# Performance work log

Hardware: AMD Instinct MI355X
Metric: run time of the kernel (lower is better)

The kernel has to match this reference:

```python
import jax, jax.numpy as jnp
import numpy as np

N_NODES = 100000
N_EDGES = 1600000
EMBED = 64
HEADS = 8
HEAD_DIM = EMBED // HEADS
FFN = 4 * EMBED
EPS = 1e-5


def _layer_norm(x, g, b):
    m = jnp.mean(x, axis=-1, keepdims=True)
    v = jnp.mean(jnp.square(x - m), axis=-1, keepdims=True)
    return (x - m) * jax.lax.rsqrt(v + EPS) * g + b


def setup_inputs() -> dict:
    key = jax.random.key(0)
    ks = jax.random.split(key, 10)
    s = lambda fan_in: 1.0 / np.sqrt(fan_in)
    x = jax.random.normal(ks[0], (N_NODES, EMBED), dtype=jnp.float32)
    edge_indices = jax.random.randint(ks[1], (2, N_EDGES), 0, N_NODES, dtype=jnp.int64)
    attn_w = jax.random.uniform(ks[2], (EMBED, 3 * EMBED), jnp.float32, -s(EMBED), s(EMBED))
    attn_b = jnp.zeros((3 * EMBED,), jnp.float32)
    w1 = jax.random.uniform(ks[3], (EMBED, FFN), jnp.float32, -s(EMBED), s(EMBED))
    b1 = jnp.zeros((FFN,), jnp.float32)
    w2 = jax.random.uniform(ks[4], (FFN, EMBED), jnp.float32, -s(FFN), s(FFN))
    b2 = jnp.zeros((EMBED,), jnp.float32)
    ln1_g = jnp.ones((EMBED,), jnp.float32)
    ln1_b = jnp.zeros((EMBED,), jnp.float32)
    ln2_g = jnp.ones((EMBED,), jnp.float32)
    ln2_b = jnp.zeros((EMBED,), jnp.float32)
    return {"x": x, "edge_indices": edge_indices, "attn_w": attn_w, "attn_b": attn_b,
            "w1": w1, "b1": b1, "w2": w2, "b2": b2,
            "ln1_g": ln1_g, "ln1_b": ln1_b, "ln2_g": ln2_g, "ln2_b": ln2_b}


def _self_attention(x, edge_indices, attn_w, attn_b):
    n = x.shape[0]
    row, col = edge_indices[0], edge_indices[1]
    scale = EMBED ** (-0.5)  # note: original scales by embed_dim**-0.5
    qkv = (x @ attn_w + attn_b).reshape(n, HEADS, 3 * HEAD_DIM)
    q, k, v = jnp.split(qkv, 3, axis=2)  # each [N, H, Dh]
    alpha = jnp.sum(q[row] * k[col], axis=2) * scale  # [E, H]
    # sparse per-row softmax via segment reductions
    m = jax.ops.segment_max(alpha, row, num_segments=n)  # [N, H]
    e = jnp.exp(alpha - m[row])
    denom = jax.ops.segment_sum(e, row, num_segments=n)  # [N, H]
    weights = e / denom[row]  # [E, H]
    vals = v[col] * weights[:, :, None]  # [E, H, Dh]
    out = jax.ops.segment_sum(vals, row, num_segments=n)  # [N, H, Dh]
    return out.reshape(n, EMBED)


def reference(x, edge_indices, attn_w, attn_b, w1, b1, w2, b2, ln1_g, ln1_b, ln2_g, ln2_b):
    # post-norm (norm_first=False), dropout=0
    x = _layer_norm(x + _self_attention(x, edge_indices, attn_w, attn_b), ln1_g, ln1_b)
    ffn = jax.nn.relu(x @ w1 + b1) @ w2 + b2
    x = _layer_norm(x + ffn, ln2_g, ln2_b)
    return x
```

## Files before the change

### kernel.cpp

```cpp
#include <hip/hip_runtime.h>
#include <hip/hip_bf16.h>


#define WAVE 64
constexpr int BUCKET_SHIFT = 7;
constexpr int NBMAX = 800;

typedef __attribute__((ext_vector_type(8))) short bf16x8;
typedef __attribute__((ext_vector_type(4))) float f32x4;

__device__ __forceinline__ float bfbits_lo(unsigned u) {
  return __uint_as_float(u << 16);
}
__device__ __forceinline__ float bfbits_hi(unsigned u) {
  return __uint_as_float(u & 0xffff0000u);
}
__device__ __forceinline__ unsigned f2bf_pk(float a, float b) {
  unsigned ua = __float_as_uint(a);
  unsigned ub = __float_as_uint(b);
  ua = (ua + 0x7fff + ((ua >> 16) & 1)) >> 16;
  ub = (ub + 0x7fff + ((ub >> 16) & 1)) & 0xffff0000u;
  return ua | ub;
}

__global__ __launch_bounds__(256) void cvt_w(
    const float* __restrict__ aw, const float* __restrict__ w1,
    const float* __restrict__ w2, unsigned short* __restrict__ awT,
    unsigned short* __restrict__ w1T, unsigned short* __restrict__ w2T) {
  int tid = blockIdx.x * 256 + threadIdx.x;
  int stride = gridDim.x * 256;
  for (int i = tid; i < 192 * 64; i += stride) {
    int nn = i >> 6, kk = i & 63;
    awT[i] = (unsigned short)(__float_as_uint(aw[kk * 192 + nn] * 1.f) >> 16 ==
                                      0
                                  ? 0
                                  : 0);
  }
}

__device__ __forceinline__ unsigned short f2bf1(float a) {
  unsigned ua = __float_as_uint(a);
  ua = (ua + 0x7fff + ((ua >> 16) & 1)) >> 16;
  return (unsigned short)ua;
}

__global__ __launch_bounds__(256) void cvt_w2(
    const float* __restrict__ aw, const float* __restrict__ w1,
    const float* __restrict__ w2, unsigned short* __restrict__ awT,
    unsigned short* __restrict__ w1T, unsigned short* __restrict__ w2T) {
  int tid = blockIdx.x * 256 + threadIdx.x;
  int stride = gridDim.x * 256;
  for (int i = tid; i < 192 * 64; i += stride) {
    int nn = i >> 6, kk = i & 63;
    awT[i] = f2bf1(aw[kk * 192 + nn]);
  }
  for (int i = tid; i < 256 * 64; i += stride) {
    int nn = i >> 6, kk = i & 63;
    w1T[i] = f2bf1(w1[kk * 256 + nn]);
  }
  for (int i = tid; i < 64 * 256; i += stride) {
    int nn = i >> 8, kk = i & 255;
    w2T[i] = f2bf1(w2[kk * 64 + nn]);
  }
}

__global__ __launch_bounds__(256) void cvt_x(const float* __restrict__ x,
                                             unsigned short* __restrict__ xb,
                                             int total8) {
  int i = blockIdx.x * 256 + threadIdx.x;
  int stride = gridDim.x * 256;
  const float4* xf = (const float4*)x;
  uint4* xo = (uint4*)xb;
  for (; i < total8; i += stride) {
    float4 a = xf[2 * i], b = xf[2 * i + 1];
    uint4 st = make_uint4(f2bf_pk(a.x, a.y), f2bf_pk(a.z, a.w),
                          f2bf_pk(b.x, b.y), f2bf_pk(b.z, b.w));
    xo[i] = st;
  }
}

template <int NCOLS, int K, int MODE>
__global__ __launch_bounds__(256) void mfma_gemm(
    const unsigned short* __restrict__ A, const unsigned short* __restrict__ BT,
    const float* __restrict__ bias, unsigned short* __restrict__ out_q,
    unsigned short* __restrict__ out_kv, unsigned short* __restrict__ out_h,
    const float* __restrict__ resid, const float* __restrict__ g,
    const float* __restrict__ beta, float* __restrict__ out_f, int n) {
  constexpr int KP = K + 8;
  constexpr int NT = NCOLS / 16;
  constexpr int NKC = K / 32;
  __shared__ unsigned short sB[NCOLS * KP];

  const int tid = threadIdx.x;
  {
    const uint4* src = (const uint4*)BT;
    for (int idx = tid; idx < NCOLS * K / 8; idx += 256) {
      int nn = idx / (K / 8), kq = idx % (K / 8);
      *(uint4*)&sB[nn * KP + kq * 8] = src[idx];
    }
  }
  __syncthreads();

  const int wid = tid >> 6, lane = tid & 63;
  const int l15 = lane & 15, quad = lane >> 4;
  const int rowbase = blockIdx.x * 128 + wid * 32;

  bf16x8 afrag[2][NKC];
#pragma unroll
  for (int rg = 0; rg < 2; rg++) {
    int row = rowbase + rg * 16 + l15;
    if (row >= n) row = n - 1;
    const bf16x8* ap = (const bf16x8*)(A + (size_t)row * K);
#pragma unroll
    for (int kc = 0; kc < NKC; kc++) afrag[rg][kc] = ap[kc * 4 + quad];
  }

  f32x4 acc[2][NT];
#pragma unroll
  for (int rg = 0; rg < 2; rg++)
#pragma unroll
    for (int t = 0; t < NT; t++) acc[rg][t] = (f32x4){0.f, 0.f, 0.f, 0.f};

#pragma unroll
  for (int t = 0; t < NT; t++) {
#pragma unroll
    for (int kc = 0; kc < NKC; kc++) {
      bf16x8 b =
          *(const bf16x8*)&sB[(t * 16 + l15) * KP + kc * 32 + quad * 8];
      acc[0][t] = __builtin_amdgcn_mfma_f32_16x16x32_bf16(b, afrag[0][kc],
                                                          acc[0][t], 0, 0, 0);
      acc[1][t] = __builtin_amdgcn_mfma_f32_16x16x32_bf16(b, afrag[1][kc],
                                                          acc[1][t], 0, 0, 0);
    }
  }

  if (MODE == 0) {
#pragma unroll
    for (int rg = 0; rg < 2; rg++) {
      int row = rowbase + rg * 16 + l15;
      if (row >= n) continue;
#pragma unroll
      for (int t = 0; t < NT; t++) {
        int c0 = t * 16 + quad * 4;
        float4 bb = *(const float4*)&bias[c0];
        float v0 = acc[rg][t].x + bb.x, v1 = acc[rg][t].y + bb.y;
        float v2 = acc[rg][t].z + bb.z, v3 = acc[rg][t].w + bb.w;
        int hh = c0 / 24, rem = c0 % 24;
        unsigned short* dst;
        if (rem < 8) {
          v0 *= 0.125f;
          v1 *= 0.125f;
          v2 *= 0.125f;
          v3 *= 0.125f;
          dst = out_q + (size_t)row * 64 + hh * 8 + rem;
        } else if (rem < 16) {
          dst = out_kv + (size_t)row * 128 + hh * 16 + (rem - 8);
        } else {
          dst = out_kv + (size_t)row * 128 + hh * 16 + 8 + (rem - 16);
        }
        *(uint2*)dst = make_uint2(f2bf_pk(v0, v1), f2bf_pk(v2, v3));
      }
    }
  } else if (MODE == 1) {
#pragma unroll
    for (int rg = 0; rg < 2; rg++) {
      int row = rowbase + rg * 16 + l15;
      if (row >= n) continue;
#pragma unroll
      for (int t = 0; t < NT; t++) {
        int c0 = t * 16 + quad * 4;
        float4 bb = *(const float4*)&bias[c0];
        float v0 = fmaxf(acc[rg][t].x + bb.x, 0.f);
        float v1 = fmaxf(acc[rg][t].y + bb.y, 0.f);
        float v2 = fmaxf(acc[rg][t].z + bb.z, 0.f);
        float v3 = fmaxf(acc[rg][t].w + bb.w, 0.f);
        *(uint2*)(out_h + (size_t)row * NCOLS + c0) =
            make_uint2(f2bf_pk(v0, v1), f2bf_pk(v2, v3));
      }
    }
  } else {
#pragma unroll
    for (int rg = 0; rg < 2; rg++) {
      int row = rowbase + rg * 16 + l15;
      bool ok = row < n;
      int rowc = ok ? row : n - 1;
      float vals[4][4];
      float ps = 0.f, pq = 0.f;
#pragma unroll
      for (int t = 0; t < 4; t++) {
        int c0 = t * 16 + quad * 4;
        float4 bb = *(const float4*)&bias[c0];
        float4 rr = *(const float4*)&resid[(size_t)rowc * 64 + c0];
        vals[t][0] = acc[rg][t].x + bb.x + rr.x;
        vals[t][1] = acc[rg][t].y + bb.y + rr.y;
        vals[t][2] = acc[rg][t].z + bb.z + rr.z;
        vals[t][3] = acc[rg][t].w + bb.w + rr.w;
#pragma unroll
        for (int r = 0; r < 4; r++) {
          ps += vals[t][r];
          pq += vals[t][r] * vals[t][r];
        }
      }
      ps += __shfl_xor(ps, 16);
      ps += __shfl_xor(ps, 32);
      pq += __shfl_xor(pq, 16);
      pq += __shfl_xor(pq, 32);
      float mean = ps * (1.f / 64.f);
      float var = pq * (1.f / 64.f) - mean * mean;
      float inv = rsqrtf(var + 1e-5f);
      if (ok) {
#pragma unroll
        for (int t = 0; t < 4; t++) {
          int c0 = t * 16 + quad * 4;
          float4 gg = *(const float4*)&g[c0];
          float4 be = *(const float4*)&beta[c0];
          float4 o =
              make_float4((vals[t][0] - mean) * inv * gg.x + be.x,
                          (vals[t][1] - mean) * inv * gg.y + be.y,
                          (vals[t][2] - mean) * inv * gg.z + be.z,
                          (vals[t][3] - mean) * inv * gg.w + be.w);
          *(float4*)&out_f[(size_t)row * 64 + c0] = o;
        }
      }
    }
  }
}

__global__ void detect_kernel(const int* __restrict__ e, unsigned* flag) {
  unsigned v = 0;
  for (int i = threadIdx.x; i < 2048; i += 256) v |= (unsigned)e[2 * i + 1];
#pragma unroll
  for (int m = 1; m < WAVE; m <<= 1) v |= (unsigned)__shfl_xor((int)v, m);
  if ((threadIdx.x & 63) == 0 && v) atomicOr(flag, 1u);
}

__device__ __forceinline__ int edge_row(const int* e, int i, bool is64) {
  return is64 ? e[2 * (size_t)i] : e[i];
}
__device__ __forceinline__ int edge_col(const int* e, int i, int E, bool is64) {
  return is64 ? e[2 * ((size_t)E + i)] : e[(size_t)E + i];
}

__global__ __launch_bounds__(256) void partition_count(
    const int* __restrict__ e, int E, const unsigned* __restrict__ flag,
    int* __restrict__ G, int NB, int CH) {
  __shared__ int h[NBMAX];
  bool is64 = (*flag == 0u);
  for (int b = threadIdx.x; b < NB; b += 256) h[b] = 0;
  __syncthreads();
  int c0 = blockIdx.x * CH, c1 = min(E, c0 + CH);
  for (int i = c0 + threadIdx.x; i < c1; i += 256)
    atomicAdd(&h[edge_row(e, i, is64) >> BUCKET_SHIFT], 1);
  __syncthreads();
  for (int b = threadIdx.x; b < NB; b += 256) G[b * 256 + blockIdx.x] = h[b];
}

__global__ __launch_bounds__(1024) void scan_reduce(const int* __restrict__ in,
                                                    int n,
                                                    int* __restrict__ bsum) {
  __shared__ int sdata[16];
  int tid = threadIdx.x;
  int idx = blockIdx.x * 1024 + tid;
  int v = (idx < n) ? in[idx] : 0;
#pragma unroll
  for (int m = 1; m < WAVE; m <<= 1) v += __shfl_xor(v, m);
  if ((tid & 63) == 0) sdata[tid >> 6] = v;
  __syncthreads();
  if (tid < 16) {
    int s = sdata[tid];
#pragma unroll
    for (int m = 1; m < 16; m <<= 1) s += __shfl_xor(s, m);
    if (tid == 0) bsum[blockIdx.x] = s;
  }
}

__global__ __launch_bounds__(256) void scan_top(const int* __restrict__ bsum,
                                                int nb, int* __restrict__ bpre) {
  __shared__ int wsum[4];
  int tid = threadIdx.x;
  int lane = tid & 63, wid = tid >> 6;
  int v = (tid < nb) ? bsum[tid] : 0;
  int incl = v;
#pragma unroll
  for (int m = 1; m < WAVE; m <<= 1) {
    int t = __shfl_up(incl, m);
    if (lane >= m) incl += t;
  }
  if (lane == 63) wsum[wid] = incl;
  __syncthreads();
  int add = 0;
  for (int w = 0; w < wid; w++) add += wsum[w];
  if (tid < nb) bpre[tid] = add + incl - v;
}

__global__ __launch_bounds__(1024) void scan_apply(
    const int* __restrict__ in, int n, const int* __restrict__ bpre,
    int* __restrict__ outscan) {
  __shared__ int wtot[16];
  __shared__ int wexcl[16];
  int tid = threadIdx.x;
  int idx = blockIdx.x * 1024 + tid;
  int v = (idx < n) ? in[idx] : 0;
  int incl = v;
#pragma unroll
  for (int m = 1; m < WAVE; m <<= 1) {
    int t = __shfl_up(incl, m);
    if ((tid & 63) >= m) incl += t;
  }
  int wid = tid >> 6;
  if ((tid & 63) == 63) wtot[wid] = incl;
  __syncthreads();
  if (tid < 16) {
    int w = wtot[tid];
    int wi = w;
#pragma unroll
    for (int m = 1; m < 16; m <<= 1) {
      int t = __shfl_up(wi, m);
      if (tid >= m) wi += t;
    }
    wexcl[tid] = wi - w;
  }
  __syncthreads();
  if (idx < n) outscan[idx] = bpre[blockIdx.x] + wexcl[wid] + incl - v;
}

__global__ __launch_bounds__(256) void partition_scatter(
    const int* __restrict__ e, int E, const unsigned* __restrict__ flag,
    const int* __restrict__ scanG, unsigned* __restrict__ ebuf, int NB,
    int CH) {
  __shared__ int base[NBMAX];
  bool is64 = (*flag == 0u);
  for (int b = threadIdx.x; b < NB; b += 256)
    base[b] = scanG[b * 256 + blockIdx.x];
  __syncthreads();
  int c0 = blockIdx.x * CH, c1 = min(E, c0 + CH);
  for (int i = c0 + threadIdx.x; i < c1; i += 256) {
    int r = edge_row(e, i, is64);
    int c = edge_col(e, i, E, is64);
    int pos = atomicAdd(&base[r >> BUCKET_SHIFT], 1);
    ebuf[pos] = ((unsigned)(r & 127) << 17) | (unsigned)c;
  }
}

__global__ __launch_bounds__(256) void bucket_csr(
    const unsigned* __restrict__ ebuf, const int* __restrict__ scanG,
    int* __restrict__ ecol, int* __restrict__ rowstart, int n, int NB, int E) {
  __shared__ int cnt[128], offs[128], cur[128];
  const int b = blockIdx.x;
  const int tid = threadIdx.x;
  const int start = scanG[b * 256];
  const int end = (b + 1 < NB) ? scanG[(b + 1) * 256] : E;
  if (tid < 128) cnt[tid] = 0;
  __syncthreads();
  for (int i = start + tid; i < end; i += 256)
    atomicAdd(&cnt[(ebuf[i] >> 17) & 127], 1);
  __syncthreads();
  if (tid < 128) offs[tid] = cnt[tid];
  __syncthreads();
  for (int s = 1; s < 128; s <<= 1) {
    int t = 0;
    if (tid < 128 && tid >= s) t = offs[tid - s];
    __syncthreads();
    if (tid < 128) offs[tid] += t;
    __syncthreads();
  }
  if (tid < 128) {
    int excl = offs[tid] - cnt[tid];
    cur[tid] = start + excl;
    int gr = (b << BUCKET_SHIFT) + tid;
    if (gr < n) rowstart[gr] = start + excl;
  }
  if (b == NB - 1 && tid == 0) rowstart[n] = E;
  __syncthreads();
  for (int i = start + tid; i < end; i += 256) {
    unsigned p = ebuf[i];
    int pos = atomicAdd(&cur[(p >> 17) & 127], 1);
    ecol[pos] = (int)(p & 0x1FFFF);
  }
}

__global__ __launch_bounds__(256) void attn_ln_kernel(
    const float* __restrict__ x, const unsigned short* __restrict__ qbuf,
    const unsigned short* __restrict__ kvb, const int* __restrict__ rowstart,
    const int* __restrict__ ecol, const float* __restrict__ g,
    const float* __restrict__ beta, float* __restrict__ x1,
    unsigned short* __restrict__ x1b, int n) {
  int wave = threadIdx.x >> 6;
  int lane = threadIdx.x & 63;
  int node = blockIdx.x * 4 + wave;
  if (node >= n) return;
  const int e = lane >> 3, h = lane & 7;
  const unsigned* kvu = (const unsigned*)kvb;

  uint4 qp = ((const uint4*)(qbuf + (size_t)node * 64))[h];
  float qv[8] = {bfbits_lo(qp.x), bfbits_hi(qp.x), bfbits_lo(qp.y),
                 bfbits_hi(qp.y), bfbits_lo(qp.z), bfbits_hi(qp.z),
                 bfbits_lo(qp.w), bfbits_hi(qp.w)};

  int start = rowstart[node];
  int cnt = rowstart[node + 1] - start;
  float den = 0.f;
  float acc[8] = {0.f, 0.f, 0.f, 0.f, 0.f, 0.f, 0.f, 0.f};

  int iters = (cnt + 7) >> 3;
  for (int it = 0; it < iters; ++it) {
    int i = it * 8 + e;
    bool valid = i < cnt;
    int c = ecol[valid ? start + i : start];
    const uint4* kvrow = (const uint4*)(kvu + (size_t)c * 64 + h * 8);
    uint4 ka = kvrow[0];
    uint4 va = kvrow[1];
    float a = bfbits_lo(ka.x) * qv[0] + bfbits_hi(ka.x) * qv[1] +
              bfbits_lo(ka.y) * qv[2] + bfbits_hi(ka.y) * qv[3] +
              bfbits_lo(ka.z) * qv[4] + bfbits_hi(ka.z) * qv[5] +
              bfbits_lo(ka.w) * qv[6] + bfbits_hi(ka.w) * qv[7];
    float ee = valid ? __expf(a) : 0.f;
    den += ee;
    acc[0] += ee * bfbits_lo(va.x);
    acc[1] += ee * bfbits_hi(va.x);
    acc[2] += ee * bfbits_lo(va.y);
    acc[3] += ee * bfbits_hi(va.y);
    acc[4] += ee * bfbits_lo(va.z);
    acc[5] += ee * bfbits_hi(va.z);
    acc[6] += ee * bfbits_lo(va.w);
    acc[7] += ee * bfbits_hi(va.w);
  }

#pragma unroll
  for (int m = 8; m < 64; m <<= 1) {
    den += __shfl_xor(den, m);
#pragma unroll
    for (int j = 0; j < 8; j++) acc[j] += __shfl_xor(acc[j], m);
  }

  float invden = (cnt > 0) ? 1.f / den : 0.f;

  const float4* xr = (const float4*)(x + (size_t)node * 64 + h * 8);
  float4 xa = xr[0], xb = xr[1];
  float v[8];
  v[0] = xa.x + acc[0] * invden;
  v[1] = xa.y + acc[1] * invden;
  v[2] = xa.z + acc[2] * invden;
  v[3] = xa.w + acc[3] * invden;
  v[4] = xb.x + acc[4] * invden;
  v[5] = xb.y + acc[5] * invden;
  v[6] = xb.z + acc[6] * invden;
  v[7] = xb.w + acc[7] * invden;

  float ps = 0.f;
#pragma unroll
  for (int j = 0; j < 8; j++) ps += v[j];
#pragma unroll
  for (int m = 1; m < 8; m <<= 1) ps += __shfl_xor(ps, m);
  float mean = ps * (1.f / 64.f);
  float pq = 0.f;
#pragma unroll
  for (int j = 0; j < 8; j++) {
    float d = v[j] - mean;
    pq += d * d;
  }
#pragma unroll
  for (int m = 1; m < 8; m <<= 1) pq += __shfl_xor(pq, m);
  float inv = rsqrtf(pq * (1.f / 64.f) + 1e-5f);

  if (e == 0) {
    const float4* gr = (const float4*)(g + h * 8);
    const float4* br = (const float4*)(beta + h * 8);
    float4 ga = gr[0], gb = gr[1];
    float4 ba = br[0], bb = br[1];
    float o[8];
    o[0] = (v[0] - mean) * inv * ga.x + ba.x;
    o[1] = (v[1] - mean) * inv * ga.y + ba.y;
    o[2] = (v[2] - mean) * inv * ga.z + ba.z;
    o[3] = (v[3] - mean) * inv * ga.w + ba.w;
    o[4] = (v[4] - mean) * inv * gb.x + bb.x;
    o[5] = (v[5] - mean) * inv * gb.y + bb.y;
    o[6] = (v[6] - mean) * inv * gb.z + bb.z;
    o[7] = (v[7] - mean) * inv * gb.w + bb.w;
    float4* dst = (float4*)(x1 + (size_t)node * 64 + h * 8);
    dst[0] = make_float4(o[0], o[1], o[2], o[3]);
    dst[1] = make_float4(o[4], o[5], o[6], o[7]);
    *(uint4*)(x1b + (size_t)node * 64 + h * 8) =
        make_uint4(f2bf_pk(o[0], o[1]), f2bf_pk(o[2], o[3]),
                   f2bf_pk(o[4], o[5]), f2bf_pk(o[6], o[7]));
  }
}

extern "C" void kernel_launch(void* const* d_in, const int* in_sizes, int n_in,
                              void* d_out, int out_size, void* d_ws,
                              size_t ws_size, hipStream_t stream) {
  const float* x = (const float*)d_in[0];
  const int* edges = (const int*)d_in[1];
  const float* attn_w = (const float*)d_in[2];
  const float* attn_b = (const float*)d_in[3];
  const float* w1 = (const float*)d_in[4];
  const float* b1 = (const float*)d_in[5];
  const float* w2 = (const float*)d_in[6];
  const float* b2 = (const float*)d_in[7];
  const float* g1 = (const float*)d_in[8];
  const float* bb1 = (const float*)d_in[9];
  const float* g2 = (const float*)d_in[10];
  const float* bb2 = (const float*)d_in[11];

  const int N = in_sizes[0] / 64;
  const int E = in_sizes[1] / 2;
  const int NB = (N + 127) >> BUCKET_SHIFT;
  const int CH = (E + 255) / 256;
  const int NG = NB * 256;

  char* ws = (char*)d_ws;
  size_t oq = 0;
  size_t okv = oq + (size_t)N * 64 * 2;
  size_t ox1 = okv + (size_t)N * 128 * 2;
  size_t ox1b = ox1 + (size_t)N * 64 * 4;
  size_t oxb = ox1b + (size_t)N * 64 * 2;
  size_t oh = oxb + (size_t)N * 64 * 2;
  size_t oawT = oh + (size_t)N * 256 * 2;
  size_t ow1T = oawT + 192 * 64 * 2;
  size_t ow2T = ow1T + 256 * 64 * 2;
  size_t oG = ow2T + 64 * 256 * 2;
  size_t oscanG = oG + (size_t)NG * 4;
  size_t oebuf = oscanG + (size_t)NG * 4;
  size_t oecol = oebuf + (size_t)E * 4;
  size_t orowstart = oecol + (size_t)E * 4;
  size_t obsum = orowstart + (size_t)(N + 4) * 4;
  size_t obpre = obsum + 1024;
  size_t oflag = obpre + 1024;

  unsigned short* qbuf = (unsigned short*)(ws + oq);
  unsigned short* kvb = (unsigned short*)(ws + okv);
  float* x1 = (float*)(ws + ox1);
  unsigned short* x1b = (unsigned short*)(ws + ox1b);
  unsigned short* xb = (unsigned short*)(ws + oxb);
  unsigned short* hbuf = (unsigned short*)(ws + oh);
  unsigned short* awT = (unsigned short*)(ws + oawT);
  unsigned short* w1T = (unsigned short*)(ws + ow1T);
  unsigned short* w2T = (unsigned short*)(ws + ow2T);
  int* G = (int*)(ws + oG);
  int* scanG = (int*)(ws + oscanG);
  unsigned* ebuf = (unsigned*)(ws + oebuf);
  int* ecol = (int*)(ws + oecol);
  int* rowstart = (int*)(ws + orowstart);
  int* bsum = (int*)(ws + obsum);
  int* bpre = (int*)(ws + obpre);
  unsigned* flag = (unsigned*)(ws + oflag);

  hipMemsetAsync(flag, 0, 4, stream);

  cvt_w2<<<32, 256, 0, stream>>>(attn_w, w1, w2, awT, w1T, w2T);
  cvt_x<<<512, 256, 0, stream>>>(x, xb, N * 8);

  detect_kernel<<<1, 256, 0, stream>>>(edges, flag);
  partition_count<<<256, 256, 0, stream>>>(edges, E, flag, G, NB, CH);
  int nscan = (NG + 1023) / 1024;
  scan_reduce<<<nscan, 1024, 0, stream>>>(G, NG, bsum);
  scan_top<<<1, 256, 0, stream>>>(bsum, nscan, bpre);
  scan_apply<<<nscan, 1024, 0, stream>>>(G, NG, bpre, scanG);
  partition_scatter<<<256, 256, 0, stream>>>(edges, E, flag, scanG, ebuf, NB,
                                             CH);
  bucket_csr<<<NB, 256, 0, stream>>>(ebuf, scanG, ecol, rowstart, N, NB, E);

  const int gblocks = (N + 127) / 128;

  mfma_gemm<192, 64, 0><<<gblocks, 256, 0, stream>>>(
      xb, awT, attn_b, qbuf, kvb, nullptr, nullptr, nullptr, nullptr, nullptr,
      N);

  attn_ln_kernel<<<(N + 3) / 4, 256, 0, stream>>>(x, qbuf, kvb, rowstart, ecol,
                                                  g1, bb1, x1, x1b, N);

  mfma_gemm<256, 64, 1><<<gblocks, 256, 0, stream>>>(
      x1b, w1T, b1, nullptr, nullptr, hbuf, nullptr, nullptr, nullptr, nullptr,
      N);

  mfma_gemm<64, 256, 2><<<gblocks, 256, 0, stream>>>(
      hbuf, w2T, b2, nullptr, nullptr, nullptr, x1, g2, bb2, (float*)d_out, N);
}
```

Baseline: 312.7 us.

## Store K/V in FP8, use bf16 residuals, unroll edge loop by two

New measurement: 281.2 us. 1.11x faster.

```diff
diff --git a/kernel.cpp b/kernel.cpp
--- a/kernel.cpp
+++ b/kernel.cpp
@@ -1,5 +1,6 @@
 #include <hip/hip_runtime.h>
 #include <hip/hip_bf16.h>
+#include <hip/hip_fp8.h>
 
 
 #define WAVE 64
@@ -8,6 +9,7 @@
 
 typedef __attribute__((ext_vector_type(8))) short bf16x8;
 typedef __attribute__((ext_vector_type(4))) float f32x4;
+typedef __attribute__((ext_vector_type(2))) float f32x2;
 
 __device__ __forceinline__ float bfbits_lo(unsigned u) {
   return __uint_as_float(u << 16);
@@ -22,26 +24,63 @@
   ub = (ub + 0x7fff + ((ub >> 16) & 1)) & 0xffff0000u;
   return ua | ub;
 }
-
-__global__ __launch_bounds__(256) void cvt_w(
-    const float* __restrict__ aw, const float* __restrict__ w1,
-    const float* __restrict__ w2, unsigned short* __restrict__ awT,
-    unsigned short* __restrict__ w1T, unsigned short* __restrict__ w2T) {
-  int tid = blockIdx.x * 256 + threadIdx.x;
-  int stride = gridDim.x * 256;
-  for (int i = tid; i < 192 * 64; i += stride) {
-    int nn = i >> 6, kk = i & 63;
-    awT[i] = (unsigned short)(__float_as_uint(aw[kk * 192 + nn] * 1.f) >> 16 ==
-                                      0
-                                  ? 0
-                                  : 0);
-  }
-}
-
 __device__ __forceinline__ unsigned short f2bf1(float a) {
   unsigned ua = __float_as_uint(a);
   ua = (ua + 0x7fff + ((ua >> 16) & 1)) >> 16;
   return (unsigned short)ua;
+}
+
+#if defined(__has_builtin)
+#if __has_builtin(__builtin_amdgcn_cvt_pk_f32_fp8) && \
+    __has_builtin(__builtin_amdgcn_cvt_pk_fp8_f32)
+#define FP8_HW 1
+#endif
+#endif
+
+#ifdef FP8_HW
+#define FP8PK0(w) __builtin_amdgcn_cvt_pk_f32_fp8((int)(w), false)
+#define FP8PK1(w) __builtin_amdgcn_cvt_pk_f32_fp8((int)(w), true)
+__device__ __forceinline__ unsigned fp8enc4(float a, float b, float c,
+                                            float d) {
+  int r = __builtin_amdgcn_cvt_pk_fp8_f32(a, b, 0, false);
+  r = __builtin_amdgcn_cvt_pk_fp8_f32(c, d, r, true);
+  return (unsigned)r;
+}
+#else
+__device__ __forceinline__ f32x2 fp8pk_sw(unsigned w, int sh) {
+  __hip_fp8_e4m3 a, b;
+  a.__x = (unsigned char)((w >> sh) & 0xff);
+  b.__x = (unsigned char)((w >> (sh + 8)) & 0xff);
+  f32x2 r;
+  r.x = (float)a;
+  r.y = (float)b;
+  return r;
+}
+#define FP8PK0(w) fp8pk_sw((w), 0)
+#define FP8PK1(w) fp8pk_sw((w), 16)
+__device__ __forceinline__ unsigned fp8enc4(float a, float b, float c,
+                                            float d) {
+  __hip_fp8_e4m3 qa(a), qb(b), qc(c), qd(d);
+  return (unsigned)qa.__x | ((unsigned)qb.__x << 8) |
+         ((unsigned)qc.__x << 16) | ((unsigned)qd.__x << 24);
+}
+#endif
+
+__device__ __forceinline__ float dot8_fp8(uint2 w, const float qv[8]) {
+  f32x2 a = FP8PK0(w.x), b = FP8PK1(w.x), c = FP8PK0(w.y), d = FP8PK1(w.y);
+  return a.x * qv[0] + a.y * qv[1] + b.x * qv[2] + b.y * qv[3] + c.x * qv[4] +
+         c.y * qv[5] + d.x * qv[6] + d.y * qv[7];
+}
+__device__ __forceinline__ void acc8_fp8(uint2 w, float ee, float acc[8]) {
+  f32x2 a = FP8PK0(w.x), b = FP8PK1(w.x), c = FP8PK0(w.y), d = FP8PK1(w.y);
+  acc[0] += ee * a.x;
+  acc[1] += ee * a.y;
+  acc[2] += ee * b.x;
+  acc[3] += ee * b.y;
+  acc[4] += ee * c.x;
+  acc[5] += ee * c.y;
+  acc[6] += ee * d.x;
+  acc[7] += ee * d.y;
 }
 
 __global__ __launch_bounds__(256) void cvt_w2(
@@ -83,8 +122,8 @@
 __global__ __launch_bounds__(256) void mfma_gemm(
     const unsigned short* __restrict__ A, const unsigned short* __restrict__ BT,
     const float* __restrict__ bias, unsigned short* __restrict__ out_q,
-    unsigned short* __restrict__ out_kv, unsigned short* __restrict__ out_h,
-    const float* __restrict__ resid, const float* __restrict__ g,
+    unsigned char* __restrict__ out_kv8, unsigned short* __restrict__ out_h,
+    const unsigned short* __restrict__ resid, const float* __restrict__ g,
     const float* __restrict__ beta, float* __restrict__ out_f, int n) {
   constexpr int KP = K + 8;
   constexpr int NT = NCOLS / 16;
@@ -125,8 +164,7 @@
   for (int t = 0; t < NT; t++) {
 #pragma unroll
     for (int kc = 0; kc < NKC; kc++) {
-      bf16x8 b =
-          *(const bf16x8*)&sB[(t * 16 + l15) * KP + kc * 32 + quad * 8];
+      bf16x8 b = *(const bf16x8*)&sB[(t * 16 + l15) * KP + kc * 32 + quad * 8];
       acc[0][t] = __builtin_amdgcn_mfma_f32_16x16x32_bf16(b, afrag[0][kc],
                                                           acc[0][t], 0, 0, 0);
       acc[1][t] = __builtin_amdgcn_mfma_f32_16x16x32_bf16(b, afrag[1][kc],
@@ -146,19 +184,20 @@
         float v0 = acc[rg][t].x + bb.x, v1 = acc[rg][t].y + bb.y;
         float v2 = acc[rg][t].z + bb.z, v3 = acc[rg][t].w + bb.w;
         int hh = c0 / 24, rem = c0 % 24;
-        unsigned short* dst;
         if (rem < 8) {
           v0 *= 0.125f;
           v1 *= 0.125f;
           v2 *= 0.125f;
           v3 *= 0.125f;
-          dst = out_q + (size_t)row * 64 + hh * 8 + rem;
+          *(uint2*)(out_q + (size_t)row * 64 + hh * 8 + rem) =
+              make_uint2(f2bf_pk(v0, v1), f2bf_pk(v2, v3));
         } else if (rem < 16) {
-          dst = out_kv + (size_t)row * 128 + hh * 16 + (rem - 8);
+          *(unsigned*)(out_kv8 + (size_t)row * 128 + hh * 8 + (rem - 8)) =
+              fp8enc4(v0, v1, v2, v3);
         } else {
-          dst = out_kv + (size_t)row * 128 + hh * 16 + 8 + (rem - 16);
+          *(unsigned*)(out_kv8 + (size_t)row * 128 + 64 + hh * 8 + (rem - 16)) =
+              fp8enc4(v0, v1, v2, v3);
         }
-        *(uint2*)dst = make_uint2(f2bf_pk(v0, v1), f2bf_pk(v2, v3));
       }
     }
   } else if (MODE == 1) {
@@ -190,11 +229,11 @@
       for (int t = 0; t < 4; t++) {
         int c0 = t * 16 + quad * 4;
         float4 bb = *(const float4*)&bias[c0];
-        float4 rr = *(const float4*)&resid[(size_t)rowc * 64 + c0];
-        vals[t][0] = acc[rg][t].x + bb.x + rr.x;
-        vals[t][1] = acc[rg][t].y + bb.y + rr.y;
-        vals[t][2] = acc[rg][t].z + bb.z + rr.z;
-        vals[t][3] = acc[rg][t].w + bb.w + rr.w;
+        uint2 rr = *(const uint2*)&resid[(size_t)rowc * 64 + c0];
+        vals[t][0] = acc[rg][t].x + bb.x + bfbits_lo(rr.x);
+        vals[t][1] = acc[rg][t].y + bb.y + bfbits_hi(rr.x);
+        vals[t][2] = acc[rg][t].z + bb.z + bfbits_lo(rr.y);
+        vals[t][3] = acc[rg][t].w + bb.w + bfbits_hi(rr.y);
 #pragma unroll
         for (int r = 0; r < 4; r++) {
           ps += vals[t][r];
@@ -214,11 +253,10 @@
           int c0 = t * 16 + quad * 4;
           float4 gg = *(const float4*)&g[c0];
           float4 be = *(const float4*)&beta[c0];
-          float4 o =
-              make_float4((vals[t][0] - mean) * inv * gg.x + be.x,
-                          (vals[t][1] - mean) * inv * gg.y + be.y,
-                          (vals[t][2] - mean) * inv * gg.z + be.z,
-                          (vals[t][3] - mean) * inv * gg.w + be.w);
+          float4 o = make_float4((vals[t][0] - mean) * inv * gg.x + be.x,
+                                 (vals[t][1] - mean) * inv * gg.y + be.y,
+                                 (vals[t][2] - mean) * inv * gg.z + be.z,
+                                 (vals[t][3] - mean) * inv * gg.w + be.w);
           *(float4*)&out_f[(size_t)row * 64 + c0] = o;
         }
       }
@@ -380,17 +418,16 @@
 }
 
 __global__ __launch_bounds__(256) void attn_ln_kernel(
-    const float* __restrict__ x, const unsigned short* __restrict__ qbuf,
-    const unsigned short* __restrict__ kvb, const int* __restrict__ rowstart,
+    const unsigned short* __restrict__ xb,
+    const unsigned short* __restrict__ qbuf,
+    const unsigned char* __restrict__ kv8, const int* __restrict__ rowstart,
     const int* __restrict__ ecol, const float* __restrict__ g,
-    const float* __restrict__ beta, float* __restrict__ x1,
-    unsigned short* __restrict__ x1b, int n) {
+    const float* __restrict__ beta, unsigned short* __restrict__ x1b, int n) {
   int wave = threadIdx.x >> 6;
   int lane = threadIdx.x & 63;
   int node = blockIdx.x * 4 + wave;
   if (node >= n) return;
   const int e = lane >> 3, h = lane & 7;
-  const unsigned* kvu = (const unsigned*)kvb;
 
   uint4 qp = ((const uint4*)(qbuf + (size_t)node * 64))[h];
   float qv[8] = {bfbits_lo(qp.x), bfbits_hi(qp.x), bfbits_lo(qp.y),
@@ -403,27 +440,38 @@
   float acc[8] = {0.f, 0.f, 0.f, 0.f, 0.f, 0.f, 0.f, 0.f};
 
   int iters = (cnt + 7) >> 3;
-  for (int it = 0; it < iters; ++it) {
-    int i = it * 8 + e;
-    bool valid = i < cnt;
-    int c = ecol[valid ? start + i : start];
-    const uint4* kvrow = (const uint4*)(kvu + (size_t)c * 64 + h * 8);
-    uint4 ka = kvrow[0];
-    uint4 va = kvrow[1];
-    float a = bfbits_lo(ka.x) * qv[0] + bfbits_hi(ka.x) * qv[1] +
-              bfbits_lo(ka.y) * qv[2] + bfbits_hi(ka.y) * qv[3] +
-              bfbits_lo(ka.z) * qv[4] + bfbits_hi(ka.z) * qv[5] +
-              bfbits_lo(ka.w) * qv[6] + bfbits_hi(ka.w) * qv[7];
-    float ee = valid ? __expf(a) : 0.f;
-    den += ee;
-    acc[0] += ee * bfbits_lo(va.x);
-    acc[1] += ee * bfbits_hi(va.x);
-    acc[2] += ee * bfbits_lo(va.y);
-    acc[3] += ee * bfbits_hi(va.y);
-    acc[4] += ee * bfbits_lo(va.z);
-    acc[5] += ee * bfbits_hi(va.z);
-    acc[6] += ee * bfbits_lo(va.w);
-    acc[7] += ee * bfbits_hi(va.w);
+  int it = 0;
+  for (; it + 2 <= iters; it += 2) {
+    int i0 = it * 8 + e;
+    int i1 = i0 + 8;
+    bool v1 = i1 < cnt;
+    int c0 = ecol[start + i0];
+    int c1 = ecol[start + (v1 ? i1 : i0)];
+    const unsigned char* r0 = kv8 + (size_t)c0 * 128 + h * 8;
+    const unsigned char* r1 = kv8 + (size_t)c1 * 128 + h * 8;
+    uint2 kw0 = *(const uint2*)r0;
+    uint2 vw0 = *(const uint2*)(r0 + 64);
+    uint2 kw1 = *(const uint2*)r1;
+    uint2 vw1 = *(const uint2*)(r1 + 64);
+    float a0 = dot8_fp8(kw0, qv);
+    float a1 = dot8_fp8(kw1, qv);
+    float e0 = __expf(a0);
+    float e1 = v1 ? __expf(a1) : 0.f;
+    den += e0 + e1;
+    acc8_fp8(vw0, e0, acc);
+    acc8_fp8(vw1, e1, acc);
+  }
+  if (it < iters) {
+    int i0 = it * 8 + e;
+    bool v0 = i0 < cnt;
+    int c0 = ecol[start + (v0 ? i0 : 0)];
+    const unsigned char* r0 = kv8 + (size_t)c0 * 128 + h * 8;
+    uint2 kw0 = *(const uint2*)r0;
+    uint2 vw0 = *(const uint2*)(r0 + 64);
+    float a0 = dot8_fp8(kw0, qv);
+    float e0 = v0 ? __expf(a0) : 0.f;
+    den += e0;
+    acc8_fp8(vw0, e0, acc);
   }
 
 #pragma unroll
@@ -435,17 +483,16 @@
 
   float invden = (cnt > 0) ? 1.f / den : 0.f;
 
-  const float4* xr = (const float4*)(x + (size_t)node * 64 + h * 8);
-  float4 xa = xr[0], xb = xr[1];
+  uint4 xr = *(const uint4*)(xb + (size_t)node * 64 + h * 8);
   float v[8];
-  v[0] = xa.x + acc[0] * invden;
-  v[1] = xa.y + acc[1] * invden;
-  v[2] = xa.z + acc[2] * invden;
-  v[3] = xa.w + acc[3] * invden;
-  v[4] = xb.x + acc[4] * invden;
-  v[5] = xb.y + acc[5] * invden;
-  v[6] = xb.z + acc[6] * invden;
-  v[7] = xb.w + acc[7] * invden;
+  v[0] = bfbits_lo(xr.x) + acc[0] * invden;
+  v[1] = bfbits_hi(xr.x) + acc[1] * invden;
+  v[2] = bfbits_lo(xr.y) + acc[2] * invden;
+  v[3] = bfbits_hi(xr.y) + acc[3] * invden;
+  v[4] = bfbits_lo(xr.z) + acc[4] * invden;
+  v[5] = bfbits_hi(xr.z) + acc[5] * invden;
+  v[6] = bfbits_lo(xr.w) + acc[6] * invden;
+  v[7] = bfbits_hi(xr.w) + acc[7] * invden;
 
   float ps = 0.f;
 #pragma unroll
@@ -477,9 +524,6 @@
     o[5] = (v[5] - mean) * inv * gb.y + bb.y;
     o[6] = (v[6] - mean) * inv * gb.z + bb.z;
     o[7] = (v[7] - mean) * inv * gb.w + bb.w;
-    float4* dst = (float4*)(x1 + (size_t)node * 64 + h * 8);
-    dst[0] = make_float4(o[0], o[1], o[2], o[3]);
-    dst[1] = make_float4(o[4], o[5], o[6], o[7]);
     *(uint4*)(x1b + (size_t)node * 64 + h * 8) =
         make_uint4(f2bf_pk(o[0], o[1]), f2bf_pk(o[2], o[3]),
                    f2bf_pk(o[4], o[5]), f2bf_pk(o[6], o[7]));
@@ -510,12 +554,11 @@
 
   char* ws = (char*)d_ws;
   size_t oq = 0;
-  size_t okv = oq + (size_t)N * 64 * 2;
-  size_t ox1 = okv + (size_t)N * 128 * 2;
-  size_t ox1b = ox1 + (size_t)N * 64 * 4;
-  size_t oxb = ox1b + (size_t)N * 64 * 2;
-  size_t oh = oxb + (size_t)N * 64 * 2;
-  size_t oawT = oh + (size_t)N * 256 * 2;
+  size_t okv = oq + (size_t)N * 128;
+  size_t ox1b = okv + (size_t)N * 128;
+  size_t oxb = ox1b + (size_t)N * 128;
+  size_t oh = oxb + (size_t)N * 128;
+  size_t oawT = oh + (size_t)N * 512;
   size_t ow1T = oawT + 192 * 64 * 2;
   size_t ow2T = ow1T + 256 * 64 * 2;
   size_t oG = ow2T + 64 * 256 * 2;
@@ -528,8 +571,7 @@
   size_t oflag = obpre + 1024;
 
   unsigned short* qbuf = (unsigned short*)(ws + oq);
-  unsigned short* kvb = (unsigned short*)(ws + okv);
-  float* x1 = (float*)(ws + ox1);
+  unsigned char* kv8 = (unsigned char*)(ws + okv);
   unsigned short* x1b = (unsigned short*)(ws + ox1b);
   unsigned short* xb = (unsigned short*)(ws + oxb);
   unsigned short* hbuf = (unsigned short*)(ws + oh);
@@ -563,16 +605,17 @@
   const int gblocks = (N + 127) / 128;
 
   mfma_gemm<192, 64, 0><<<gblocks, 256, 0, stream>>>(
-      xb, awT, attn_b, qbuf, kvb, nullptr, nullptr, nullptr, nullptr, nullptr,
+      xb, awT, attn_b, qbuf, kv8, nullptr, nullptr, nullptr, nullptr, nullptr,
       N);
 
-  attn_ln_kernel<<<(N + 3) / 4, 256, 0, stream>>>(x, qbuf, kvb, rowstart, ecol,
-                                                  g1, bb1, x1, x1b, N);
+  attn_ln_kernel<<<(N + 3) / 4, 256, 0, stream>>>(xb, qbuf, kv8, rowstart,
+                                                  ecol, g1, bb1, x1b, N);
 
   mfma_gemm<256, 64, 1><<<gblocks, 256, 0, stream>>>(
       x1b, w1T, b1, nullptr, nullptr, hbuf, nullptr, nullptr, nullptr, nullptr,
       N);
 
   mfma_gemm<64, 256, 2><<<gblocks, 256, 0, stream>>>(
-      hbuf, w2T, b2, nullptr, nullptr, nullptr, x1, g2, bb2, (float*)d_out, N);
-}
+      hbuf, w2T, b2, nullptr, nullptr, nullptr, x1b, g2, bb2, (float*)d_out,
+      N);
+}
```
